# Optimization experiments

Measured on AMD Instinct MI355X. Metric: run time of the kernel, lower is better.

Reference implementation:

```python
import jax, jax.numpy as jnp
import numpy as np

N = 50000        # nodes per node type
E_ADJ = 800000   # edges per adjacency
E_DEC = 200000   # decoder edge batch
F = 128          # input feature dim
H = 64           # hidden dim (all hid_dims equal)
RT_NUM = 4       # DEDICOM relation subtypes
# relation order per stage: [(0,0),(0,1),(1,0),(1,1)]; input node type j per relation:
J_ORDER = (0, 1, 0, 1)


def setup_inputs() -> dict:
    key = jax.random.key(0)
    ks = jax.random.split(key, 16)
    inp = {
        'adj_rows': jax.random.randint(ks[0], (8, E_ADJ), 0, N, dtype=jnp.int32),
        'adj_cols': jax.random.randint(ks[1], (8, E_ADJ), 0, N, dtype=jnp.int32),
        'adj_vals': jax.random.uniform(ks[2], (8, E_ADJ), dtype=jnp.float32),
        'feat0': jax.random.normal(ks[3], (N, F), dtype=jnp.float32),
        'feat1': jax.random.normal(ks[4], (N, F), dtype=jnp.float32),
        'W1': jax.random.normal(ks[5], (4, F, H), dtype=jnp.float32) * 0.05,
        'W2': jax.random.normal(ks[6], (4, H, H), dtype=jnp.float32) * 0.05,
        'W3': jax.random.normal(ks[7], (4, H, H), dtype=jnp.float32) * 0.05,
        'W4': jax.random.normal(ks[8], (4, H, H), dtype=jnp.float32) * 0.05,
        'R_global': jax.random.normal(ks[9], (H, H), dtype=jnp.float32) * 0.05,
        'D_local': jax.random.normal(ks[10], (RT_NUM, H), dtype=jnp.float32) * 0.05,
        'edges': jax.random.randint(ks[11], (E_DEC, 2), 0, N, dtype=jnp.int32),
        'rt_k': 1,
    }
    return inp


def _gcn_stage(rows, cols, vals, x0, x1, W):
    """One multi-relation GCN layer over 4 relations [(0,0),(0,1),(1,0),(1,1)].
    rows/cols/vals: [4, E]; x0/x1: [N, Fin]; W: [4, Fin, H].
    Returns (out0, out1): per-destination-type summed, relu'd embeddings [N, H]."""
    xin = jnp.stack([x0, x1, x0, x1])                    # [4, N, Fin] per J_ORDER
    xw = jnp.einsum('knf,kfh->knh', xin, W)              # transform per relation

    def spmm(r, c, v, m):
        # sparse adj @ m : gather messages along cols, scatter-add into rows
        return jax.ops.segment_sum(m[c] * v[:, None], r, num_segments=N)

    y = jax.vmap(spmm)(rows, cols, vals, xw)             # [4, N, H]
    y = jax.nn.relu(y)                                   # activation inside each layer
    # get_embed: sum per-relation outputs grouped by destination type i
    return y[0] + y[1], y[2] + y[3]


def reference(adj_rows, adj_cols, adj_vals, feat0, feat1, W1, W2, W3, W4,
              R_global, D_local, edges, rt_k):
    r1, c1, v1 = adj_rows[:4], adj_cols[:4], adj_vals[:4]   # stage-1 adjacencies
    r2, c2, v2 = adj_rows[4:], adj_cols[4:], adj_vals[4:]   # stage-2 adjacencies

    h0, h1 = _gcn_stage(r1, c1, v1, feat0, feat1, W1)       # s1_l1
    h0, h1 = _gcn_stage(r1, c1, v1, h0, h1, W2)             # s1_l2
    h0, h1 = _gcn_stage(r2, c2, v2, h0, h1, W3)             # s2_l1
    h0, h1 = _gcn_stage(r2, c2, v2, h0, h1, W4)             # s2_l2

    # TDDecoder for rel_type = (0, 1): gather endpoints, DEDICOM bilinear score.
    er = h0[edges[:, 0]]                                    # [E, H]
    ec = h1[edges[:, 1]]                                    # [E, H]
    d = D_local[rt_k]                                       # [H]
    M = d[:, None] * R_global * d[None, :]                  # D_k R D_k
    # torch.diag(er @ M @ ec.T) == per-edge bilinear form
    preds_pos = jnp.einsum('eh,hg,eg->e', er, M, ec)        # [E]
    return preds_pos
```

## Files before the change

kernel.cpp:

```cpp
#include <hip/hip_runtime.h>

#define N_NODES 50000
#define E_ADJ   800000
#define E_DEC   200000
#define FDIM    128
#define HDIM    64
#define NP1     (N_NODES + 1)
#define NBUK    196
#define SUBS    32
#define SCAP    192
#define BCAP    (SUBS * SCAP)
#define TILE_E  1024
#define EPB     4
#define NPBLK   782

typedef _Float16 f16;
typedef __attribute__((ext_vector_type(2))) _Float16 f16x2;
typedef __attribute__((ext_vector_type(4))) _Float16 f16x4;
typedef __attribute__((ext_vector_type(8))) _Float16 f16x8;
typedef __attribute__((ext_vector_type(4))) float f32x4;

__device__ __forceinline__ int   ntl_i(const int* p)   { return __builtin_nontemporal_load(p); }
__device__ __forceinline__ float ntl_f(const float* p) { return __builtin_nontemporal_load(p); }

__global__ void part_kernel(const int* __restrict__ rows,
                            const int* __restrict__ cols,
                            const float* __restrict__ vals,
                            int* __restrict__ gcur,
                            unsigned long long* __restrict__ bucketed)
{
    const int k   = blockIdx.y;
    const int sub = blockIdx.x & (SUBS - 1);
    const int tid = threadIdx.x;
    const long long t0 = (long long)blockIdx.x * TILE_E;

    __shared__ int hist[NBUK];
    __shared__ int cur[NBUK];
    for (int i = tid; i < NBUK; i += 256) hist[i] = 0;
    __syncthreads();

    for (int it = 0; it < EPB; ++it) {
        const long long e = t0 + it * 256 + tid;
        if (e < E_ADJ) {
            const int r = rows[(size_t)k * E_ADJ + e];
            atomicAdd(&hist[r >> 8], 1);
        }
    }
    __syncthreads();

    for (int i = tid; i < NBUK; i += 256)
        cur[i] = (hist[i] > 0) ? atomicAdd(&gcur[(k * NBUK + i) * SUBS + sub], hist[i]) : 0;
    __syncthreads();

    for (int it = 0; it < EPB; ++it) {
        const long long e = t0 + it * 256 + tid;
        if (e < E_ADJ) {
            const int r = rows[(size_t)k * E_ADJ + e];
            const int b = r >> 8;
            const int pos = atomicAdd(&cur[b], 1);
            const int c = ntl_i(&cols[(size_t)k * E_ADJ + e]);
            const float v = ntl_f(&vals[(size_t)k * E_ADJ + e]);
            const unsigned meta = (unsigned)c | ((unsigned)(r & 255) << 16);
            const unsigned long long payload =
                ((unsigned long long)__float_as_uint(v) << 32) | meta;
            bucketed[(size_t)(k * NBUK + b) * BCAP + sub * SCAP + pos] = payload;
        }
    }
}

__global__ void bucket_scan(const int* __restrict__ gcur, int* __restrict__ srtbase)
{
    __shared__ int tot[4 * NBUK];
    for (int i = threadIdx.x; i < 4 * NBUK; i += 256) {
        int t = 0;
#pragma unroll
        for (int s8 = 0; s8 < SUBS; ++s8) t += gcur[i * SUBS + s8];
        tot[i] = t;
    }
    __syncthreads();
    if (threadIdx.x < 4) {
        const int k = threadIdx.x;
        int run = 0;
        for (int b = 0; b < NBUK; ++b) {
            srtbase[k * NBUK + b] = run;
            run += tot[k * NBUK + b];
        }
    }
}

__global__ void bucket_sort(const unsigned long long* __restrict__ bucketed,
                            const int* __restrict__ gcur,
                            const int* __restrict__ srtbase,
                            unsigned* __restrict__ srt,
                            int* __restrict__ row_ptr)
{
    const int b = blockIdx.x, k = blockIdx.y, tid = threadIdx.x;
    const int base = srtbase[k * NBUK + b];
    const unsigned long long* bk = bucketed + (size_t)(k * NBUK + b) * BCAP;

    __shared__ int scnt[SUBS];
    __shared__ int s[256];
    __shared__ int cur[256];
    __shared__ int rcnt[256];
    rcnt[tid] = 0;
    if (tid < SUBS) scnt[tid] = gcur[(k * NBUK + b) * SUBS + tid];
    __syncthreads();

    for (int s8 = 0; s8 < SUBS; ++s8) {
        const int c8 = scnt[s8];
        for (int i = tid; i < c8; i += 256) {
            const unsigned meta = (unsigned)bk[s8 * SCAP + i];
            atomicAdd(&rcnt[(meta >> 16) & 255], 1);
        }
    }
    __syncthreads();

    const int v = rcnt[tid];
    s[tid] = v;
    __syncthreads();
    for (int off = 1; off < 256; off <<= 1) {
        const int t = (tid >= off) ? s[tid - off] : 0;
        __syncthreads();
        s[tid] += t;
        __syncthreads();
    }
    const int excl = s[tid] - v;

    const int n = b * 256 + tid;
    if (n < N_NODES) row_ptr[k * NP1 + n] = base + excl;
    if (b == NBUK - 1 && tid == 0) row_ptr[k * NP1 + N_NODES] = E_ADJ;
    cur[tid] = base + excl;
    __syncthreads();

    for (int s8 = 0; s8 < SUBS; ++s8) {
        const int c8 = scnt[s8];
        for (int i = tid; i < c8; i += 256) {
            const unsigned long long p = bk[s8 * SCAP + i];
            const unsigned meta = (unsigned)p;
            const int rl = (meta >> 16) & 255;
            const int c  = meta & 0xFFFF;
            const float val = __uint_as_float((unsigned)(p >> 32));
            union { f16 h; unsigned short us; } cv;
            cv.h = (f16)val;
            const int pos = atomicAdd(&cur[rl], 1);
            srt[(size_t)k * E_ADJ + pos] = ((unsigned)cv.us << 16) | (unsigned)c;
        }
    }
}

__device__ __forceinline__ void gather_octs(const unsigned* __restrict__ sp,
                                            int s, int en,
                                            const f16* __restrict__ xk,
                                            int lane, float a[8])
{
    const int es = lane >> 3;
    const int hb = (lane & 7) * 8;

    for (int base = s; base < en; base += 64) {
        const int cnt = min(64, en - base);
        unsigned meta = 0;
        if (lane < cnt) meta = sp[base + lane];
        const int no = (cnt + 7) >> 3;
        for (int p = 0; p < no; p += 2) {
            const unsigned m0 = __shfl(meta, p * 8 + es, 64);
            const unsigned m1 = __shfl(meta, (p + 1) * 8 + es, 64);
            union { unsigned short us; f16 h; } c0, c1;
            c0.us = (unsigned short)(m0 >> 16);
            c1.us = (unsigned short)(m1 >> 16);
            const float v0 = (float)c0.h;
            const float v1 = (float)c1.h;
            const f16x8 g0 = *(const f16x8*)(xk + (size_t)(m0 & 0xFFFF) * HDIM + hb);
            const f16x8 g1 = *(const f16x8*)(xk + (size_t)(m1 & 0xFFFF) * HDIM + hb);
#pragma unroll
            for (int j = 0; j < 8; ++j)
                a[j] = fmaf((float)g0[j], v0, a[j]);
#pragma unroll
            for (int j = 0; j < 8; ++j)
                a[j] = fmaf((float)g1[j], v1, a[j]);
        }
    }
#pragma unroll
    for (int j = 0; j < 8; ++j) {
        a[j] += __shfl_xor(a[j], 8, 64);
        a[j] += __shfl_xor(a[j], 16, 64);
        a[j] += __shfl_xor(a[j], 32, 64);
    }
}

__global__ void pack_wfrag(const float* __restrict__ W, const int K,
                           f16* __restrict__ out)
{
    const int idx = blockIdx.x * 256 + threadIdx.x;
    const int j    = idx & 7;
    const int lane = (idx >> 3) & 63;
    const int kcs  = K >> 5;
    int rest = idx >> 9;
    const int kc  = rest % kcs; rest /= kcs;
    const int nt  = rest & 3;
    const int rel = rest >> 2;
    const int k   = kc * 32 + ((lane >> 4) * 8) + j;
    const int col = nt * 16 + (lane & 15);
    out[idx] = (f16)W[((size_t)rel * K + k) * HDIM + col];
}

__global__ void gemm1_mfma(const float* __restrict__ x0,
                           const float* __restrict__ x1,
                           const f16* __restrict__ wf,
                           f16* __restrict__ xw)
{
    const int wave = threadIdx.x >> 6;
    const int lane = threadIdx.x & 63;
    const int n0 = blockIdx.x * 32;
    const int q = lane >> 4, r16 = lane & 15;

    const float* xr = (wave & 1) ? x1 : x0;

    f16x8 b[4][4];
#pragma unroll
    for (int nt = 0; nt < 4; ++nt)
#pragma unroll
        for (int kc = 0; kc < 4; ++kc)
            b[nt][kc] = *(const f16x8*)(wf + (((size_t)(wave * 4 + nt) * 4 + kc) * 64 + lane) * 8);

    for (int t = 0; t < 2; ++t) {
        const int row = n0 + t * 16 + r16;
        const int rowc = row < N_NODES ? row : N_NODES - 1;
        f16x8 a[4];
#pragma unroll
        for (int kc = 0; kc < 4; ++kc) {
            const float4 lo = *(const float4*)(xr + (size_t)rowc * FDIM + kc * 32 + q * 8);
            const float4 hi = *(const float4*)(xr + (size_t)rowc * FDIM + kc * 32 + q * 8 + 4);
            f16x8 av;
            av[0] = (f16)lo.x; av[1] = (f16)lo.y; av[2] = (f16)lo.z; av[3] = (f16)lo.w;
            av[4] = (f16)hi.x; av[5] = (f16)hi.y; av[6] = (f16)hi.z; av[7] = (f16)hi.w;
            a[kc] = av;
        }
#pragma unroll
        for (int nt = 0; nt < 4; ++nt) {
            f32x4 acc = {0.f, 0.f, 0.f, 0.f};
#pragma unroll
            for (int kc = 0; kc < 4; ++kc)
                acc = __builtin_amdgcn_mfma_f32_16x16x32_f16(a[kc], b[nt][kc], acc, 0, 0, 0);
#pragma unroll
            for (int j = 0; j < 4; ++j) {
                const int n = n0 + t * 16 + q * 4 + j;
                if (n < N_NODES)
                    xw[((size_t)wave * N_NODES + n) * HDIM + nt * 16 + r16] = (f16)acc[j];
            }
        }
    }
}

__global__ void gemm2_mfma(const f16* __restrict__ agg,
                           const f16* __restrict__ wf,
                           f16* __restrict__ h0, f16* __restrict__ h1)
{
    const int wave = threadIdx.x >> 6;
    const int lane = threadIdx.x & 63;
    const int tid  = threadIdx.x;
    const int n0 = blockIdx.x * 32;
    const int q = lane >> 4, r16 = lane & 15;

    f16x8 b[4][2];
#pragma unroll
    for (int nt = 0; nt < 4; ++nt)
#pragma unroll
        for (int kc = 0; kc < 2; ++kc)
            b[nt][kc] = *(const f16x8*)(wf + (((size_t)(wave * 4 + nt) * 2 + kc) * 64 + lane) * 8);

    __shared__ f16 yt[4][16][HDIM];

    for (int t = 0; t < 2; ++t) {
        const int row = n0 + t * 16 + r16;
        const int rowc = row < N_NODES ? row : N_NODES - 1;
        f16x8 a[2];
#pragma unroll
        for (int kc = 0; kc < 2; ++kc)
            a[kc] = *(const f16x8*)(agg + ((size_t)wave * N_NODES + rowc) * HDIM + kc * 32 + q * 8);

#pragma unroll
        for (int nt = 0; nt < 4; ++nt) {
            f32x4 acc = {0.f, 0.f, 0.f, 0.f};
#pragma unroll
            for (int kc = 0; kc < 2; ++kc)
                acc = __builtin_amdgcn_mfma_f32_16x16x32_f16(a[kc], b[nt][kc], acc, 0, 0, 0);
#pragma unroll
            for (int j = 0; j < 4; ++j)
                yt[wave][q * 4 + j][nt * 16 + r16] = (f16)fmaxf(acc[j], 0.f);
        }
        __syncthreads();

        {
            const int r  = tid >> 4;
            const int c4 = (tid & 15) * 4;
            const int n  = n0 + t * 16 + r;
            if (n < N_NODES) {
                const f16x4 a0 = *(const f16x4*)&yt[0][r][c4];
                const f16x4 a1 = *(const f16x4*)&yt[1][r][c4];
                const f16x4 a2 = *(const f16x4*)&yt[2][r][c4];
                const f16x4 a3 = *(const f16x4*)&yt[3][r][c4];
                f16x4 o0, o1;
#pragma unroll
                for (int u = 0; u < 4; ++u) {
                    o0[u] = (f16)((float)a0[u] + (float)a1[u]);
                    o1[u] = (f16)((float)a2[u] + (float)a3[u]);
                }
                *(f16x4*)(h0 + (size_t)n * HDIM + c4) = o0;
                *(f16x4*)(h1 + (size_t)n * HDIM + c4) = o1;
            }
        }
        __syncthreads();
    }
}

__global__ void spmm_csr(const unsigned* __restrict__ srt,
                         const int*    __restrict__ row_ptr,
                         const f16*    __restrict__ xw,
                         f16* __restrict__ y)
{
    const int b = blockIdx.x, k = b & 3, g = b >> 2;
    const int wave = threadIdx.x >> 6, lane = threadIdx.x & 63;
    const int n = g * 4 + wave;

    const int s  = row_ptr[k * NP1 + n];
    const int en = row_ptr[k * NP1 + n + 1];
    float a[8] = {0.f, 0.f, 0.f, 0.f, 0.f, 0.f, 0.f, 0.f};
    gather_octs(srt + (size_t)k * E_ADJ, s, en,
                xw + (size_t)k * N_NODES * HDIM, lane, a);
    if (lane < 8) {
        f16x8 o;
#pragma unroll
        for (int j = 0; j < 8; ++j)
            o[j] = (f16)fmaxf(a[j], 0.f);
        *(f16x8*)(y + ((size_t)k * N_NODES + n) * HDIM + lane * 8) = o;
    }
}

__global__ void combine_kernel(const f16* __restrict__ y,
                               f16* __restrict__ h0, f16* __restrict__ h1)
{
    const size_t NHh = (size_t)N_NODES * HDIM / 2;
    const size_t i = (size_t)blockIdx.x * 256 + threadIdx.x;
    const f16x2 a = ((const f16x2*)y)[i];
    const f16x2 b = ((const f16x2*)y)[NHh + i];
    const f16x2 c = ((const f16x2*)y)[2 * NHh + i];
    const f16x2 d = ((const f16x2*)y)[3 * NHh + i];
    f16x2 o0, o1;
    o0.x = (f16)((float)a.x + (float)b.x);
    o0.y = (f16)((float)a.y + (float)b.y);
    o1.x = (f16)((float)c.x + (float)d.x);
    o1.y = (f16)((float)c.y + (float)d.y);
    ((f16x2*)h0)[i] = o0;
    ((f16x2*)h1)[i] = o1;
}

__global__ void agg_csr(const unsigned* __restrict__ srt,
                        const int*    __restrict__ row_ptr,
                        const f16*    __restrict__ h0,
                        const f16*    __restrict__ h1,
                        f16* __restrict__ agg)
{
    const int b = blockIdx.x, k = b & 3, g = b >> 2;
    const int wave = threadIdx.x >> 6, lane = threadIdx.x & 63;
    const int n = g * 4 + wave;

    const int s  = row_ptr[k * NP1 + n];
    const int en = row_ptr[k * NP1 + n + 1];
    const f16* xk = (k & 1) ? h1 : h0;
    float a[8] = {0.f, 0.f, 0.f, 0.f, 0.f, 0.f, 0.f, 0.f};
    gather_octs(srt + (size_t)k * E_ADJ, s, en, xk, lane, a);
    if (lane < 8) {
        f16x8 o;
#pragma unroll
        for (int j = 0; j < 8; ++j)
            o[j] = (f16)a[j];
        *(f16x8*)(agg + ((size_t)k * N_NODES + n) * HDIM + lane * 8) = o;
    }
}

__global__ void make_M(const float* __restrict__ R, const float* __restrict__ Dl,
                       const int* __restrict__ rt_k, float* __restrict__ M)
{
    const int i = blockIdx.x * blockDim.x + threadIdx.x;
    if (i >= HDIM * HDIM) return;
    const float* d = Dl + rt_k[0] * HDIM;
    M[i] = d[i >> 6] * R[i] * d[i & 63];
}

__global__ void h0M_kernel(const f16* __restrict__ h0, const float* __restrict__ M,
                           f16* __restrict__ A)
{
    const int wave = threadIdx.x >> 6, lane = threadIdx.x & 63;
    const int n0 = blockIdx.x * 16;

    __shared__ float sx[16][HDIM];
    for (int i = threadIdx.x; i < 16 * HDIM; i += 256)
        sx[i >> 6][i & 63] = (float)h0[(size_t)n0 * HDIM + i];
    __syncthreads();

    float acc[4] = {0.f, 0.f, 0.f, 0.f};
#pragma unroll 4
    for (int f = 0; f < HDIM; ++f) {
        const float w = M[f * HDIM + lane];
#pragma unroll
        for (int r = 0; r < 4; ++r)
            acc[r] = fmaf(sx[wave * 4 + r][f], w, acc[r]);
    }
#pragma unroll
    for (int r = 0; r < 4; ++r)
        A[(size_t)(n0 + wave * 4 + r) * HDIM + lane] = (f16)acc[r];
}

__global__ void decode(const f16* __restrict__ A, const f16* __restrict__ h1,
                       const int* __restrict__ edges, float* __restrict__ out)
{
    const int w = (blockIdx.x * 256 + threadIdx.x) >> 6;
    const int lane = threadIdx.x & 63;
    const int e = w * 4 + (lane >> 4);
    const int q = lane & 15;

    const int i = edges[2 * (size_t)e];
    const int j = edges[2 * (size_t)e + 1];

    const f16x4 a = *(const f16x4*)(A + (size_t)i * HDIM + q * 4);
    const f16x4 b = *(const f16x4*)(h1 + (size_t)j * HDIM + q * 4);
    float p = 0.f;
#pragma unroll
    for (int u = 0; u < 4; ++u)
        p = fmaf((float)a[u], (float)b[u], p);
    p += __shfl_xor(p, 1, 64);
    p += __shfl_xor(p, 2, 64);
    p += __shfl_xor(p, 4, 64);
    p += __shfl_xor(p, 8, 64);
    if (q == 0) out[e] = p;
}

static void build_csr(const int* rows, const int* cols, const float* vals,
                      int* gcur, int* srtbase, unsigned long long* bucketed,
                      unsigned* srt, int* row_ptr, hipStream_t stream)
{
    hipMemsetAsync(gcur, 0, 4 * NBUK * SUBS * sizeof(int), stream);
    part_kernel<<<dim3(NPBLK, 4), 256, 0, stream>>>(rows, cols, vals, gcur, bucketed);
    bucket_scan<<<1, 256, 0, stream>>>(gcur, srtbase);
    bucket_sort<<<dim3(NBUK, 4), 256, 0, stream>>>(bucketed, gcur, srtbase, srt, row_ptr);
}

extern "C" void kernel_launch(void* const* d_in, const int* in_sizes, int n_in,
                              void* d_out, int out_size, void* d_ws, size_t ws_size,
                              hipStream_t stream) {
    const int*   adj_rows = (const int*)  d_in[0];
    const int*   adj_cols = (const int*)  d_in[1];
    const float* adj_vals = (const float*)d_in[2];
    const float* feat0    = (const float*)d_in[3];
    const float* feat1    = (const float*)d_in[4];
    const float* W1       = (const float*)d_in[5];
    const float* W2       = (const float*)d_in[6];
    const float* W3       = (const float*)d_in[7];
    const float* W4       = (const float*)d_in[8];
    const float* Rg       = (const float*)d_in[9];
    const float* Dl       = (const float*)d_in[10];
    const int*   edges    = (const int*)  d_in[11];
    const int*   rt_k     = (const int*)  d_in[12];
    float* out = (float*)d_out;

    const size_t NH = (size_t)N_NODES * HDIM;
    float* ws = (float*)d_ws;
    f16*      xwh     = (f16*)ws;
    f16*      h0      = (f16*)(ws + 2 * NH);
    f16*      h1      = (f16*)(ws + 2 * NH + NH / 2);
    unsigned* srt     = (unsigned*)(ws + 3 * NH);
    int*      row_ptr = (int*)(ws + 3 * NH + 8 * (size_t)E_ADJ);
    int*      gcur    = row_ptr + 4 * NP1 + 60;
    int*      srtbase = gcur + 4 * NBUK * SUBS;
    float*    M       = (float*)(srtbase + 4 * NBUK + 32);
    unsigned long long* bucketed =
        (unsigned long long*)(M + HDIM * HDIM + 64);
    f16* y = (f16*)bucketed;
    f16* wfrag = (f16*)(bucketed + (size_t)4 * NBUK * BCAP);
    f16* wf1 = wfrag;
    f16* wf2 = wfrag + 32768;
    f16* wf3 = wfrag + 49152;
    f16* wf4 = wfrag + 65536;

    const int* r2 = adj_rows + 4 * (size_t)E_ADJ;
    const int* c2 = adj_cols + 4 * (size_t)E_ADJ;
    const float* v2 = adj_vals + 4 * (size_t)E_ADJ;

    pack_wfrag<<<128, 256, 0, stream>>>(W1, FDIM, wf1);
    pack_wfrag<<<64, 256, 0, stream>>>(W2, HDIM, wf2);
    pack_wfrag<<<64, 256, 0, stream>>>(W3, HDIM, wf3);
    pack_wfrag<<<64, 256, 0, stream>>>(W4, HDIM, wf4);

    build_csr(adj_rows, adj_cols, adj_vals, gcur, srtbase, bucketed, srt, row_ptr, stream);

    gemm1_mfma<<<1563, 256, 0, stream>>>(feat0, feat1, wf1, xwh);
    spmm_csr<<<N_NODES, 256, 0, stream>>>(srt, row_ptr, xwh, y);
    combine_kernel<<<(int)(NH / 2 / 256), 256, 0, stream>>>(y, h0, h1);

    agg_csr<<<N_NODES, 256, 0, stream>>>(srt, row_ptr, h0, h1, xwh);
    gemm2_mfma<<<1563, 256, 0, stream>>>(xwh, wf2, h0, h1);

    build_csr(r2, c2, v2, gcur, srtbase, bucketed, srt, row_ptr, stream);

    agg_csr<<<N_NODES, 256, 0, stream>>>(srt, row_ptr, h0, h1, xwh);
    gemm2_mfma<<<1563, 256, 0, stream>>>(xwh, wf3, h0, h1);

    agg_csr<<<N_NODES, 256, 0, stream>>>(srt, row_ptr, h0, h1, xwh);
    gemm2_mfma<<<1563, 256, 0, stream>>>(xwh, wf4, h0, h1);

    make_M<<<(HDIM * HDIM + 255) / 256, 256, 0, stream>>>(Rg, Dl, rt_k, M);
    f16* A = xwh;
    h0M_kernel<<<N_NODES / 16, 256, 0, stream>>>(h0, M, A);
    decode<<<E_DEC * 16 / 256, 256, 0, stream>>>(A, h1, edges, out);
}
```

Before: 560.4 us.

## Split CSR gathers into two column halves to shrink gather working set

The bucket sort now orders each row's edges by whether the column index falls in the lower or upper half of nodes, and records a per-row midpoint. Each SpMM/aggregation is then run as two passes, one per column half, with the second pass adding to the first pass's partial result (and applying relu at the end). The aim is to halve the source-feature working set per pass so gathers hit in L2/MALL more often. In exchange it doubles launches and per-row overhead and adds a read-modify-write of the output. It also unrolls the gather loop to four in-flight loads and uses nontemporal loads for edge metadata.

```diff
diff --git a/kernel.cpp b/kernel.cpp
--- a/kernel.cpp
+++ b/kernel.cpp
@@ -13,6 +13,7 @@
 #define TILE_E  1024
 #define EPB     4
 #define NPBLK   782
+#define COLH    25000
 
 typedef _Float16 f16;
 typedef __attribute__((ext_vector_type(2))) _Float16 f16x2;
@@ -20,8 +21,9 @@
 typedef __attribute__((ext_vector_type(8))) _Float16 f16x8;
 typedef __attribute__((ext_vector_type(4))) float f32x4;
 
-__device__ __forceinline__ int   ntl_i(const int* p)   { return __builtin_nontemporal_load(p); }
-__device__ __forceinline__ float ntl_f(const float* p) { return __builtin_nontemporal_load(p); }
+__device__ __forceinline__ int      ntl_i(const int* p)      { return __builtin_nontemporal_load(p); }
+__device__ __forceinline__ float    ntl_f(const float* p)    { return __builtin_nontemporal_load(p); }
+__device__ __forceinline__ unsigned ntl_u(const unsigned* p) { return __builtin_nontemporal_load(p); }
 
 __global__ void part_kernel(const int* __restrict__ rows,
                             const int* __restrict__ cols,
@@ -92,17 +94,19 @@
                             const int* __restrict__ gcur,
                             const int* __restrict__ srtbase,
                             unsigned* __restrict__ srt,
-                            int* __restrict__ row_ptr)
+                            int* __restrict__ row_ptr,
+                            int* __restrict__ mid)
 {
     const int b = blockIdx.x, k = blockIdx.y, tid = threadIdx.x;
     const int base = srtbase[k * NBUK + b];
     const unsigned long long* bk = bucketed + (size_t)(k * NBUK + b) * BCAP;
 
     __shared__ int scnt[SUBS];
+    __shared__ int rcnt[256][2];
     __shared__ int s[256];
-    __shared__ int cur[256];
-    __shared__ int rcnt[256];
-    rcnt[tid] = 0;
+    __shared__ int cur2[256][2];
+    rcnt[tid][0] = 0;
+    rcnt[tid][1] = 0;
     if (tid < SUBS) scnt[tid] = gcur[(k * NBUK + b) * SUBS + tid];
     __syncthreads();
 
@@ -110,13 +114,13 @@
         const int c8 = scnt[s8];
         for (int i = tid; i < c8; i += 256) {
             const unsigned meta = (unsigned)bk[s8 * SCAP + i];
-            atomicAdd(&rcnt[(meta >> 16) & 255], 1);
-        }
-    }
-    __syncthreads();
-
-    const int v = rcnt[tid];
-    s[tid] = v;
+            atomicAdd(&rcnt[(meta >> 16) & 255][(meta & 0xFFFF) >= COLH], 1);
+        }
+    }
+    __syncthreads();
+
+    const int tot = rcnt[tid][0] + rcnt[tid][1];
+    s[tid] = tot;
     __syncthreads();
     for (int off = 1; off < 256; off <<= 1) {
         const int t = (tid >= off) ? s[tid - off] : 0;
@@ -124,12 +128,16 @@
         s[tid] += t;
         __syncthreads();
     }
-    const int excl = s[tid] - v;
+    const int excl = s[tid] - tot;
 
     const int n = b * 256 + tid;
-    if (n < N_NODES) row_ptr[k * NP1 + n] = base + excl;
+    if (n < N_NODES) {
+        row_ptr[k * NP1 + n] = base + excl;
+        mid[k * N_NODES + n] = base + excl + rcnt[tid][0];
+    }
     if (b == NBUK - 1 && tid == 0) row_ptr[k * NP1 + N_NODES] = E_ADJ;
-    cur[tid] = base + excl;
+    cur2[tid][0] = base + excl;
+    cur2[tid][1] = base + excl + rcnt[tid][0];
     __syncthreads();
 
     for (int s8 = 0; s8 < SUBS; ++s8) {
@@ -142,13 +150,13 @@
             const float val = __uint_as_float((unsigned)(p >> 32));
             union { f16 h; unsigned short us; } cv;
             cv.h = (f16)val;
-            const int pos = atomicAdd(&cur[rl], 1);
+            const int pos = atomicAdd(&cur2[rl][c >= COLH], 1);
             srt[(size_t)k * E_ADJ + pos] = ((unsigned)cv.us << 16) | (unsigned)c;
         }
     }
 }
 
-__device__ __forceinline__ void gather_octs(const unsigned* __restrict__ sp,
+__device__ __forceinline__ void gather_oct4(const unsigned* __restrict__ sp,
                                             int s, int en,
                                             const f16* __restrict__ xk,
                                             int lane, float a[8])
@@ -159,24 +167,27 @@
     for (int base = s; base < en; base += 64) {
         const int cnt = min(64, en - base);
         unsigned meta = 0;
-        if (lane < cnt) meta = sp[base + lane];
+        if (lane < cnt) meta = ntl_u(&sp[base + lane]);
         const int no = (cnt + 7) >> 3;
-        for (int p = 0; p < no; p += 2) {
-            const unsigned m0 = __shfl(meta, p * 8 + es, 64);
-            const unsigned m1 = __shfl(meta, (p + 1) * 8 + es, 64);
-            union { unsigned short us; f16 h; } c0, c1;
-            c0.us = (unsigned short)(m0 >> 16);
-            c1.us = (unsigned short)(m1 >> 16);
-            const float v0 = (float)c0.h;
-            const float v1 = (float)c1.h;
-            const f16x8 g0 = *(const f16x8*)(xk + (size_t)(m0 & 0xFFFF) * HDIM + hb);
-            const f16x8 g1 = *(const f16x8*)(xk + (size_t)(m1 & 0xFFFF) * HDIM + hb);
-#pragma unroll
-            for (int j = 0; j < 8; ++j)
-                a[j] = fmaf((float)g0[j], v0, a[j]);
-#pragma unroll
-            for (int j = 0; j < 8; ++j)
-                a[j] = fmaf((float)g1[j], v1, a[j]);
+        for (int p = 0; p < no; p += 4) {
+            unsigned m[4];
+#pragma unroll
+            for (int u = 0; u < 4; ++u)
+                m[u] = __shfl(meta, (p + u) * 8 + es, 64);
+            f16x8 g[4];
+            float v[4];
+#pragma unroll
+            for (int u = 0; u < 4; ++u) {
+                union { unsigned short us; f16 h; } cv;
+                cv.us = (unsigned short)(m[u] >> 16);
+                v[u] = (float)cv.h;
+                g[u] = *(const f16x8*)(xk + (size_t)(m[u] & 0xFFFF) * HDIM + hb);
+            }
+#pragma unroll
+            for (int u = 0; u < 4; ++u)
+#pragma unroll
+                for (int j = 0; j < 8; ++j)
+                    a[j] = fmaf((float)g[u][j], v[u], a[j]);
         }
     }
 #pragma unroll
@@ -184,6 +195,43 @@
         a[j] += __shfl_xor(a[j], 8, 64);
         a[j] += __shfl_xor(a[j], 16, 64);
         a[j] += __shfl_xor(a[j], 32, 64);
+    }
+}
+
+template <int MODE, int ADD, int RELU>
+__global__ void gather_half(const unsigned* __restrict__ srt,
+                            const int*    __restrict__ row_ptr,
+                            const int*    __restrict__ mid,
+                            const f16*    __restrict__ t0,
+                            const f16*    __restrict__ t1,
+                            f16* __restrict__ outb)
+{
+    const int b = blockIdx.x, k = b & 3, g = b >> 2;
+    const int wave = threadIdx.x >> 6, lane = threadIdx.x & 63;
+    const int n = g * 4 + wave;
+
+    int s, en;
+    if (!ADD) { s = row_ptr[k * NP1 + n]; en = mid[k * N_NODES + n]; }
+    else      { s = mid[k * N_NODES + n]; en = row_ptr[k * NP1 + n + 1]; }
+
+    const f16* xk = (MODE == 0) ? (t0 + (size_t)k * N_NODES * HDIM)
+                                : ((k & 1) ? t1 : t0);
+
+    float a[8] = {0.f, 0.f, 0.f, 0.f, 0.f, 0.f, 0.f, 0.f};
+    gather_oct4(srt + (size_t)k * E_ADJ, s, en, xk, lane, a);
+
+    if (lane < 8) {
+        f16* dst = outb + ((size_t)k * N_NODES + n) * HDIM + lane * 8;
+        if (ADD) {
+            const f16x8 pr = *(const f16x8*)dst;
+#pragma unroll
+            for (int j = 0; j < 8; ++j) a[j] += (float)pr[j];
+        }
+        f16x8 o;
+#pragma unroll
+        for (int j = 0; j < 8; ++j)
+            o[j] = RELU ? (f16)fmaxf(a[j], 0.f) : (f16)a[j];
+        *(f16x8*)dst = o;
     }
 }
 
@@ -310,29 +358,6 @@
             }
         }
         __syncthreads();
-    }
-}
-
-__global__ void spmm_csr(const unsigned* __restrict__ srt,
-                         const int*    __restrict__ row_ptr,
-                         const f16*    __restrict__ xw,
-                         f16* __restrict__ y)
-{
-    const int b = blockIdx.x, k = b & 3, g = b >> 2;
-    const int wave = threadIdx.x >> 6, lane = threadIdx.x & 63;
-    const int n = g * 4 + wave;
-
-    const int s  = row_ptr[k * NP1 + n];
-    const int en = row_ptr[k * NP1 + n + 1];
-    float a[8] = {0.f, 0.f, 0.f, 0.f, 0.f, 0.f, 0.f, 0.f};
-    gather_octs(srt + (size_t)k * E_ADJ, s, en,
-                xw + (size_t)k * N_NODES * HDIM, lane, a);
-    if (lane < 8) {
-        f16x8 o;
-#pragma unroll
-        for (int j = 0; j < 8; ++j)
-            o[j] = (f16)fmaxf(a[j], 0.f);
-        *(f16x8*)(y + ((size_t)k * N_NODES + n) * HDIM + lane * 8) = o;
     }
 }
 
@@ -354,30 +379,6 @@
     ((f16x2*)h1)[i] = o1;
 }
 
-__global__ void agg_csr(const unsigned* __restrict__ srt,
-                        const int*    __restrict__ row_ptr,
-                        const f16*    __restrict__ h0,
-                        const f16*    __restrict__ h1,
-                        f16* __restrict__ agg)
-{
-    const int b = blockIdx.x, k = b & 3, g = b >> 2;
-    const int wave = threadIdx.x >> 6, lane = threadIdx.x & 63;
-    const int n = g * 4 + wave;
-
-    const int s  = row_ptr[k * NP1 + n];
-    const int en = row_ptr[k * NP1 + n + 1];
-    const f16* xk = (k & 1) ? h1 : h0;
-    float a[8] = {0.f, 0.f, 0.f, 0.f, 0.f, 0.f, 0.f, 0.f};
-    gather_octs(srt + (size_t)k * E_ADJ, s, en, xk, lane, a);
-    if (lane < 8) {
-        f16x8 o;
-#pragma unroll
-        for (int j = 0; j < 8; ++j)
-            o[j] = (f16)a[j];
-        *(f16x8*)(agg + ((size_t)k * N_NODES + n) * HDIM + lane * 8) = o;
-    }
-}
-
 __global__ void make_M(const float* __restrict__ R, const float* __restrict__ Dl,
                        const int* __restrict__ rt_k, float* __restrict__ M)
 {
@@ -437,12 +438,12 @@
 
 static void build_csr(const int* rows, const int* cols, const float* vals,
                       int* gcur, int* srtbase, unsigned long long* bucketed,
-                      unsigned* srt, int* row_ptr, hipStream_t stream)
+                      unsigned* srt, int* row_ptr, int* mid, hipStream_t stream)
 {
     hipMemsetAsync(gcur, 0, 4 * NBUK * SUBS * sizeof(int), stream);
     part_kernel<<<dim3(NPBLK, 4), 256, 0, stream>>>(rows, cols, vals, gcur, bucketed);
     bucket_scan<<<1, 256, 0, stream>>>(gcur, srtbase);
-    bucket_sort<<<dim3(NBUK, 4), 256, 0, stream>>>(bucketed, gcur, srtbase, srt, row_ptr);
+    bucket_sort<<<dim3(NBUK, 4), 256, 0, stream>>>(bucketed, gcur, srtbase, srt, row_ptr, mid);
 }
 
 extern "C" void kernel_launch(void* const* d_in, const int* in_sizes, int n_in,
@@ -472,7 +473,8 @@
     int*      row_ptr = (int*)(ws + 3 * NH + 8 * (size_t)E_ADJ);
     int*      gcur    = row_ptr + 4 * NP1 + 60;
     int*      srtbase = gcur + 4 * NBUK * SUBS;
-    float*    M       = (float*)(srtbase + 4 * NBUK + 32);
+    int*      mid     = srtbase + 4 * NBUK + 32;
+    float*    M       = (float*)(mid + 4 * N_NODES + 32);
     unsigned long long* bucketed =
         (unsigned long long*)(M + HDIM * HDIM + 64);
     f16* y = (f16*)bucketed;
@@ -491,21 +493,25 @@
     pack_wfrag<<<64, 256, 0, stream>>>(W3, HDIM, wf3);
     pack_wfrag<<<64, 256, 0, stream>>>(W4, HDIM, wf4);
 
-    build_csr(adj_rows, adj_cols, adj_vals, gcur, srtbase, bucketed, srt, row_ptr, stream);
+    build_csr(adj_rows, adj_cols, adj_vals, gcur, srtbase, bucketed, srt, row_ptr, mid, stream);
 
     gemm1_mfma<<<1563, 256, 0, stream>>>(feat0, feat1, wf1, xwh);
-    spmm_csr<<<N_NODES, 256, 0, stream>>>(srt, row_ptr, xwh, y);
+    gather_half<0, 0, 0><<<N_NODES, 256, 0, stream>>>(srt, row_ptr, mid, xwh, xwh, y);
+    gather_half<0, 1, 1><<<N_NODES, 256, 0, stream>>>(srt, row_ptr, mid, xwh, xwh, y);
     combine_kernel<<<(int)(NH / 2 / 256), 256, 0, stream>>>(y, h0, h1);
 
-    agg_csr<<<N_NODES, 256, 0, stream>>>(srt, row_ptr, h0, h1, xwh);
+    gather_half<1, 0, 0><<<N_NODES, 256, 0, stream>>>(srt, row_ptr, mid, h0, h1, xwh);
+    gather_half<1, 1, 0><<<N_NODES, 256, 0, stream>>>(srt, row_ptr, mid, h0, h1, xwh);
     gemm2_mfma<<<1563, 256, 0, stream>>>(xwh, wf2, h0, h1);
 
-    build_csr(r2, c2, v2, gcur, srtbase, bucketed, srt, row_ptr, stream);
-
-    agg_csr<<<N_NODES, 256, 0, stream>>>(srt, row_ptr, h0, h1, xwh);
+    build_csr(r2, c2, v2, gcur, srtbase, bucketed, srt, row_ptr, mid, stream);
+
+    gather_half<1, 0, 0><<<N_NODES, 256, 0, stream>>>(srt, row_ptr, mid, h0, h1, xwh);
+    gather_half<1, 1, 0><<<N_NODES, 256, 0, stream>>>(srt, row_ptr, mid, h0, h1, xwh);
     gemm2_mfma<<<1563, 256, 0, stream>>>(xwh, wf3, h0, h1);
 
-    agg_csr<<<N_NODES, 256, 0, stream>>>(srt, row_ptr, h0, h1, xwh);
+    gather_half<1, 0, 0><<<N_NODES, 256, 0, stream>>>(srt, row_ptr, mid, h0, h1, xwh);
+    gather_half<1, 1, 0><<<N_NODES, 256, 0, stream>>>(srt, row_ptr, mid, h0, h1, xwh);
     gemm2_mfma<<<1563, 256, 0, stream>>>(xwh, wf4, h0, h1);
 
     make_M<<<(HDIM * HDIM + 255) / 256, 256, 0, stream>>>(Rg, Dl, rt_k, M);
```

Measured after the change: 876.0 us. 1.56x slower.
